# Optimization experiments

Hardware: AMD Instinct MI355X
Metric: run time of the kernel (lower is better)

## Reference

```python
import jax, jax.numpy as jnp
import numpy as np

N_NODES = 100000


def _gcn_norm(edge_index, num_nodes):
    # PyG GCNConv default: add self-loops, symmetric normalization.
    src = jnp.concatenate([edge_index[0], jnp.arange(num_nodes, dtype=edge_index.dtype)])
    dst = jnp.concatenate([edge_index[1], jnp.arange(num_nodes, dtype=edge_index.dtype)])
    deg = jax.ops.segment_sum(jnp.ones_like(dst, dtype=jnp.float32), dst, num_segments=num_nodes)
    dis = jnp.where(deg > 0, jax.lax.rsqrt(deg), 0.0)  # deg^{-1/2}
    norm = dis[src] * dis[dst]  # [E + N]
    return src, dst, norm


def _gcn_conv(x, W, b, src, dst, norm, num_nodes):
    h = x @ W.T                      # [N, out] transform first (out < in)
    msg = h[src] * norm[:, None]     # gather + per-edge scale
    agg = jax.ops.segment_sum(msg, dst, num_segments=num_nodes)  # scatter-add
    return agg + b


def setup_inputs() -> dict:
    key = jax.random.key(0)
    ks = jax.random.split(key, 12)
    E = 3200000
    x = jax.random.normal(ks[0], (N_NODES, 128), dtype=jnp.float32)
    edge_index = jax.random.randint(ks[1], (2, E), 0, N_NODES, dtype=jnp.int64)
    s = lambda k, sh, fan: jax.random.normal(k, sh, dtype=jnp.float32) * (1.0 / np.sqrt(fan))
    return {
        "x": x,
        "edge_index": edge_index,
        "W1": s(ks[2], (32, 128), 128), "b1": jnp.zeros((32,), jnp.float32),
        "W2": s(ks[3], (16, 32), 32),   "b2": jnp.zeros((16,), jnp.float32),
        "w_ih": s(ks[4], (32, 16), 16), "w_hh": s(ks[5], (32, 8), 8),
        "b_ih": s(ks[6], (32,), 8),     "b_hh": s(ks[7], (32,), 8),
        "W_out": s(ks[8], (1, 8), 8),   "b_out": jnp.zeros((1,), jnp.float32),
    }


def reference(x, edge_index, W1, b1, W2, b2, w_ih, w_hh, b_ih, b_hh, W_out, b_out):
    src, dst, norm = _gcn_norm(edge_index, N_NODES)
    h = jax.nn.relu(_gcn_conv(x, W1, b1, src, dst, norm, N_NODES))   # [N, 32]
    h = jax.nn.relu(_gcn_conv(h, W2, b2, src, dst, norm, N_NODES))   # [N, 16]
    # Single-timestep LSTM with h0 = c0 = 0 (gate order: i, f, g, o).
    gates = h @ w_ih.T + b_ih + b_hh   # [N, 32]; h0 @ w_hh.T term is zero
    i, f, g, o = jnp.split(gates, 4, axis=-1)
    c = jax.nn.sigmoid(i) * jnp.tanh(g)
    hh = jax.nn.sigmoid(o) * jnp.tanh(c)  # [N, 8]
    out = hh @ W_out.T + b_out            # [N, 1]
    return out.squeeze(-1)                # [N]
```

## Files before the change

### kernel.cpp

```cpp
#include <hip/hip_runtime.h>
#include <hip/hip_fp16.h>
#include <math.h>

static constexpr int N = 100000;
static constexpr int SHIFT = 7;
static constexpr int BUCKN = 1 << SHIFT;
static constexpr int NBUCK = (N + BUCKN - 1) >> SHIFT;
static constexpr int CHUNK = 12288;
static constexpr int STRIDE = 5120;
static constexpr int COLCAP = NBUCK * STRIDE;

__global__ __launch_bounds__(1024) void k_init(int* __restrict__ gcur) {
    int b = threadIdx.x;
    if (b < NBUCK) gcur[b] = b * STRIDE;
}

__global__ __launch_bounds__(1024) void k_part(const int* __restrict__ src,
                                               const int* __restrict__ dst,
                                               int* __restrict__ gcur,
                                               int* __restrict__ col, int E) {
    __shared__ int ss[CHUNK];
    __shared__ int ds[CHUNK];
    __shared__ int hl[NBUCK];
    __shared__ int cur[NBUCK];
    const int t = threadIdx.x, b = blockIdx.x;
    if (t < NBUCK) hl[t] = 0;
    __syncthreads();
    const int e0 = b * CHUNK;
    const int m = min(CHUNK, E - e0);
    for (int i = t; i < m; i += 1024) {
        int d = dst[e0 + i], s = src[e0 + i];
        ss[i] = s;
        ds[i] = d;
        atomicAdd(&hl[d >> SHIFT], 1);
    }
    __syncthreads();
    if (t < NBUCK) cur[t] = atomicAdd(&gcur[t], hl[t]);
    __syncthreads();
    for (int i = t; i < m; i += 1024) {
        int d = ds[i];
        int pos = atomicAdd(&cur[d >> SHIFT], 1);
        pos = min(max(pos, 0), COLCAP - 1);
        col[pos] = (ss[i] & 0x1FFFF) | ((d & (BUCKN - 1)) << 17);
    }
}

__global__ __launch_bounds__(1024) void k_sort(const int* __restrict__ gcur,
                                               int* __restrict__ col,
                                               int* __restrict__ deg,
                                               int* __restrict__ row_start) {
    __shared__ int es[STRIDE];
    __shared__ int cnt[BUCKN];
    __shared__ int cur[BUCKN];
    const int t = threadIdx.x, buck = blockIdx.x;
    const int s0 = buck * STRIDE;
    int n = gcur[buck] - s0;
    n = max(0, min(n, STRIDE));
    if (t < BUCKN) cnt[t] = 0;
    __syncthreads();
    for (int i = t; i < n; i += 1024) {
        int p = col[s0 + i];
        es[i] = p;
        atomicAdd(&cnt[(p >> 17) & (BUCKN - 1)], 1);
    }
    __syncthreads();
    if (t < BUCKN) cur[t] = cnt[t];
    __syncthreads();
    for (int off = 1; off < BUCKN; off <<= 1) {
        int v = (t < BUCKN && t >= off) ? cur[t - off] : 0;
        __syncthreads();
        if (t < BUCKN) cur[t] += v;
        __syncthreads();
    }
    if (t < BUCKN) {
        int excl = cur[t] - cnt[t];
        int node = buck * BUCKN + t;
        if (node < N) {
            deg[node] = cnt[t];
            row_start[node] = s0 + excl;
        }
        cur[t] = excl;
    }
    __syncthreads();
    for (int i = t; i < n; i += 1024) {
        int p = es[i];
        int pos = atomicAdd(&cur[(p >> 17) & (BUCKN - 1)], 1);
        pos = min(max(pos, 0), STRIDE - 1);
        col[s0 + pos] = p & 0x1FFFF;
    }
}

__global__ __launch_bounds__(256) void k_xw1(
        const float* __restrict__ x, const float* __restrict__ W1,
        const int* __restrict__ deg, __half* __restrict__ g1h) {
    __shared__ float4 wtv[32 * 33];
    __shared__ float4 xsv[1024];
    const int t = threadIdx.x;
    const float4* W1v = (const float4*)W1;
    for (int idx = t; idx < 1024; idx += 256) {
        int j = idx >> 5, kb = idx & 31;
        wtv[kb * 33 + j] = W1v[idx];
    }
    const float4* x4 = (const float4*)x + (size_t)blockIdx.x * 1024;
    for (int idx = t; idx < 1024; idx += 256) xsv[idx] = x4[idx];
    __syncthreads();

    const int j = t & 31, ng = t >> 5;
    float a0 = 0.f, a1 = 0.f, a2 = 0.f, a3 = 0.f;
#pragma unroll 4
    for (int kb = 0; kb < 32; ++kb) {
        float4 w = wtv[kb * 33 + j];
        float4 x0 = xsv[(4 * ng + 0) * 32 + kb];
        float4 x1 = xsv[(4 * ng + 1) * 32 + kb];
        float4 x2 = xsv[(4 * ng + 2) * 32 + kb];
        float4 x3 = xsv[(4 * ng + 3) * 32 + kb];
        a0 = fmaf(w.x, x0.x, fmaf(w.y, x0.y, fmaf(w.z, x0.z, fmaf(w.w, x0.w, a0))));
        a1 = fmaf(w.x, x1.x, fmaf(w.y, x1.y, fmaf(w.z, x1.z, fmaf(w.w, x1.w, a1))));
        a2 = fmaf(w.x, x2.x, fmaf(w.y, x2.y, fmaf(w.z, x2.z, fmaf(w.w, x2.w, a2))));
        a3 = fmaf(w.x, x3.x, fmaf(w.y, x3.y, fmaf(w.z, x3.z, fmaf(w.w, x3.w, a3))));
    }
    const int nb = blockIdx.x * 32 + 4 * ng;
    g1h[(nb + 0) * 32 + j] = __float2half(a0 * rsqrtf((float)(deg[nb + 0] + 1)));
    g1h[(nb + 1) * 32 + j] = __float2half(a1 * rsqrtf((float)(deg[nb + 1] + 1)));
    g1h[(nb + 2) * 32 + j] = __float2half(a2 * rsqrtf((float)(deg[nb + 2] + 1)));
    g1h[(nb + 3) * 32 + j] = __float2half(a3 * rsqrtf((float)(deg[nb + 3] + 1)));
}

__global__ __launch_bounds__(256) void k_gather1(
        const int* __restrict__ row_start, const int* __restrict__ deg,
        const int* __restrict__ col, const __half* __restrict__ g1h,
        const float* __restrict__ b1, const float* __restrict__ W2,
        __half* __restrict__ g2h) {
    __shared__ float h1s[64 * 33];
    __shared__ float w2t[32 * 17];
    const int t = threadIdx.x;
    for (int idx = t; idx < 512; idx += 256) {
        int j = idx >> 5, k = idx & 31;
        w2t[k * 17 + j] = W2[idx];
    }
    const int lane = t & 63, w = t >> 6;
    const int q = lane & 3;
    const int nloc = w * 16 + (lane >> 2);
    const int node = blockIdx.x * 64 + nloc;
    const int nc = node < N ? node : N - 1;
    const int rs = row_start[nc];
    const int ne = (node < N) ? deg[nc] : 0;
    const uint4* g1v = (const uint4*)g1h;

    float acc[8];
    {
        uint4 rv = g1v[nc * 4 + q];
        const __half2* hp = (const __half2*)&rv;
#pragma unroll
        for (int m2 = 0; m2 < 4; ++m2) {
            float2 f = __half22float2(hp[m2]);
            acc[2 * m2] = f.x;
            acc[2 * m2 + 1] = f.y;
        }
    }
    for (int base = 0; base < ne; base += 16) {
        int sv[4];
#pragma unroll
        for (int c = 0; c < 4; ++c)
            sv[c] = (base + 4 * c + q < ne) ? col[rs + base + 4 * c + q] : 0;
        int idx[16];
#pragma unroll
        for (int c = 0; c < 4; ++c)
#pragma unroll
            for (int u = 0; u < 4; ++u)
                idx[4 * c + u] = min(__shfl(sv[c], u, 4), N - 1);
        uint4 rv[16];
#pragma unroll
        for (int u = 0; u < 16; ++u) rv[u] = g1v[idx[u] * 4 + q];
#pragma unroll
        for (int u = 0; u < 16; ++u) {
            float wt = (base + u < ne) ? 1.f : 0.f;
            const __half2* hp = (const __half2*)&rv[u];
#pragma unroll
            for (int m2 = 0; m2 < 4; ++m2) {
                float2 f = __half22float2(hp[m2]);
                acc[2 * m2]     = fmaf(wt, f.x, acc[2 * m2]);
                acc[2 * m2 + 1] = fmaf(wt, f.y, acc[2 * m2 + 1]);
            }
        }
    }
    {
        const float dis = rsqrtf((float)(ne + 1));
#pragma unroll
        for (int u = 0; u < 8; ++u) {
            float v = (node < N) ? (acc[u] * dis + b1[q * 8 + u]) : 0.f;
            h1s[nloc * 33 + q * 8 + u] = v > 0.f ? v : 0.f;
        }
    }
    __syncthreads();
    const int n2 = t >> 2, jq = (t & 3) * 4;
    const int node2 = blockIdx.x * 64 + n2;
    if (node2 < N) {
        float a0 = 0.f, a1 = 0.f, a2 = 0.f, a3 = 0.f;
        const float* hr = h1s + n2 * 33;
#pragma unroll
        for (int k = 0; k < 32; ++k) {
            float h = hr[k];
            a0 = fmaf(h, w2t[k * 17 + jq + 0], a0);
            a1 = fmaf(h, w2t[k * 17 + jq + 1], a1);
            a2 = fmaf(h, w2t[k * 17 + jq + 2], a2);
            a3 = fmaf(h, w2t[k * 17 + jq + 3], a3);
        }
        const float dis2 = rsqrtf((float)(deg[node2] + 1));
        __half2* g2p = (__half2*)(g2h + node2 * 16 + jq);
        g2p[0] = __floats2half2_rn(a0 * dis2, a1 * dis2);
        g2p[1] = __floats2half2_rn(a2 * dis2, a3 * dis2);
    }
}

__global__ __launch_bounds__(256) void k_gather2(
        const int* __restrict__ row_start, const int* __restrict__ deg,
        const int* __restrict__ col, const __half* __restrict__ g2h,
        const float* __restrict__ b2, float* __restrict__ h2) {
    const int t = threadIdx.x;
    const int lane = t & 63, w = t >> 6;
    const int q = lane & 1;
    const int node = blockIdx.x * 128 + w * 32 + (lane >> 1);
    const int nc = node < N ? node : N - 1;
    const int rs = row_start[nc];
    const int ne = (node < N) ? deg[nc] : 0;
    const uint4* g2v = (const uint4*)g2h;

    float acc[8];
    {
        uint4 rv = g2v[nc * 2 + q];
        const __half2* hp = (const __half2*)&rv;
#pragma unroll
        for (int m2 = 0; m2 < 4; ++m2) {
            float2 f = __half22float2(hp[m2]);
            acc[2 * m2] = f.x;
            acc[2 * m2 + 1] = f.y;
        }
    }
    for (int base = 0; base < ne; base += 16) {
        int sv[8];
#pragma unroll
        for (int c = 0; c < 8; ++c)
            sv[c] = (base + 2 * c + q < ne) ? col[rs + base + 2 * c + q] : 0;
        int idx[16];
#pragma unroll
        for (int c = 0; c < 8; ++c) {
            idx[2 * c]     = min(__shfl(sv[c], 0, 2), N - 1);
            idx[2 * c + 1] = min(__shfl(sv[c], 1, 2), N - 1);
        }
        uint4 rv[16];
#pragma unroll
        for (int u = 0; u < 16; ++u) rv[u] = g2v[idx[u] * 2 + q];
#pragma unroll
        for (int u = 0; u < 16; ++u) {
            float wt = (base + u < ne) ? 1.f : 0.f;
            const __half2* hp = (const __half2*)&rv[u];
#pragma unroll
            for (int m2 = 0; m2 < 4; ++m2) {
                float2 f = __half22float2(hp[m2]);
                acc[2 * m2]     = fmaf(wt, f.x, acc[2 * m2]);
                acc[2 * m2 + 1] = fmaf(wt, f.y, acc[2 * m2 + 1]);
            }
        }
    }
    if (node < N) {
        const float dis = rsqrtf((float)(ne + 1));
        float4* h2v = (float4*)h2;
#pragma unroll
        for (int h = 0; h < 2; ++h) {
            float4 o;
            float v0 = acc[4 * h + 0] * dis + b2[q * 8 + 4 * h + 0];
            float v1 = acc[4 * h + 1] * dis + b2[q * 8 + 4 * h + 1];
            float v2 = acc[4 * h + 2] * dis + b2[q * 8 + 4 * h + 2];
            float v3 = acc[4 * h + 3] * dis + b2[q * 8 + 4 * h + 3];
            o.x = v0 > 0.f ? v0 : 0.f;
            o.y = v1 > 0.f ? v1 : 0.f;
            o.z = v2 > 0.f ? v2 : 0.f;
            o.w = v3 > 0.f ? v3 : 0.f;
            h2v[node * 4 + q * 2 + h] = o;
        }
    }
}

__global__ __launch_bounds__(256) void k_final(
        const float* __restrict__ h2g,
        const float* __restrict__ w_ih, const float* __restrict__ b_ih,
        const float* __restrict__ b_hh, const float* __restrict__ W_out,
        const float* __restrict__ b_out, float* __restrict__ out) {
    __shared__ float wih[512];
    __shared__ float bias[32];
    __shared__ float wout[8];
    __shared__ float bo;
    const int t = threadIdx.x;
    for (int idx = t; idx < 512; idx += 256) wih[idx] = w_ih[idx];
    if (t < 32) bias[t] = b_ih[t] + b_hh[t];
    if (t < 8)  wout[t] = W_out[t];
    if (t == 0) bo = b_out[0];
    __syncthreads();

    const int i = blockIdx.x * 256 + t;
    if (i >= N) return;
    float h2[16];
    const float4* a4 = (const float4*)(h2g + (size_t)i * 16);
#pragma unroll
    for (int q = 0; q < 4; ++q) {
        float4 v = a4[q];
        h2[q * 4 + 0] = v.x; h2[q * 4 + 1] = v.y;
        h2[q * 4 + 2] = v.z; h2[q * 4 + 3] = v.w;
    }
    float oacc = 0.f;
#pragma unroll
    for (int q = 0; q < 8; ++q) {
        float gi = bias[q], gg = bias[16 + q], go = bias[24 + q];
#pragma unroll
        for (int k = 0; k < 16; ++k) {
            gi = fmaf(h2[k], wih[q * 16 + k], gi);
            gg = fmaf(h2[k], wih[(16 + q) * 16 + k], gg);
            go = fmaf(h2[k], wih[(24 + q) * 16 + k], go);
        }
        float c  = (1.f / (1.f + expf(-gi))) * tanhf(gg);
        float hh = (1.f / (1.f + expf(-go))) * tanhf(c);
        oacc = fmaf(hh, wout[q], oacc);
    }
    out[i] = oacc + bo;
}

extern "C" void kernel_launch(void* const* d_in, const int* in_sizes, int n_in,
                              void* d_out, int out_size, void* d_ws, size_t ws_size,
                              hipStream_t stream) {
    const float* x     = (const float*)d_in[0];
    const int*   ei    = (const int*)d_in[1];
    const float* W1    = (const float*)d_in[2];
    const float* b1    = (const float*)d_in[3];
    const float* W2    = (const float*)d_in[4];
    const float* b2    = (const float*)d_in[5];
    const float* w_ih  = (const float*)d_in[6];
    const float* b_ih  = (const float*)d_in[8];
    const float* b_hh  = (const float*)d_in[9];
    const float* W_out = (const float*)d_in[10];
    const float* b_out = (const float*)d_in[11];
    float* out = (float*)d_out;

    const int E = in_sizes[1] / 2;
    const int* src = ei;
    const int* dst = ei + E;
    const int BP = (E + CHUNK - 1) / CHUNK;

    int* col       = (int*)d_ws;
    int* deg       = col + COLCAP;
    int* row_start = deg + N;
    int* gcur      = row_start + N;
    int* base2     = gcur + 784;
    __half* g1h    = (__half*)base2;
    __half* g2h    = (__half*)(base2 + (size_t)N * 16);
    float* h2      = (float*)(base2 + (size_t)N * 24);

    k_init   <<<1,               1024, 0, stream>>>(gcur);
    k_part   <<<BP,              1024, 0, stream>>>(src, dst, gcur, col, E);
    k_sort   <<<NBUCK,           1024, 0, stream>>>(gcur, col, deg, row_start);
    k_xw1    <<<N / 32,          256,  0, stream>>>(x, W1, deg, g1h);
    k_gather1<<<(N + 63) / 64,   256,  0, stream>>>(row_start, deg, col, g1h, b1, W2, g2h);
    k_gather2<<<(N + 127) / 128, 256,  0, stream>>>(row_start, deg, col, g2h, b2, h2);
    k_final  <<<(N + 255) / 256, 256,  0, stream>>>(h2, w_ih, b_ih, b_hh, W_out, b_out, out);
}
```

Measured before the change: 264.2 us.

## Fuse LSTM head into second gather and stream partition reads from global

```diff
diff --git a/kernel.cpp b/kernel.cpp
--- a/kernel.cpp
+++ b/kernel.cpp
@@ -6,7 +6,7 @@
 static constexpr int SHIFT = 7;
 static constexpr int BUCKN = 1 << SHIFT;
 static constexpr int NBUCK = (N + BUCKN - 1) >> SHIFT;
-static constexpr int CHUNK = 12288;
+static constexpr int CHUNK = 16384;
 static constexpr int STRIDE = 5120;
 static constexpr int COLCAP = NBUCK * STRIDE;
 
@@ -19,8 +19,6 @@
                                                const int* __restrict__ dst,
                                                int* __restrict__ gcur,
                                                int* __restrict__ col, int E) {
-    __shared__ int ss[CHUNK];
-    __shared__ int ds[CHUNK];
     __shared__ int hl[NBUCK];
     __shared__ int cur[NBUCK];
     const int t = threadIdx.x, b = blockIdx.x;
@@ -28,20 +26,15 @@
     __syncthreads();
     const int e0 = b * CHUNK;
     const int m = min(CHUNK, E - e0);
+    for (int i = t; i < m; i += 1024) atomicAdd(&hl[dst[e0 + i] >> SHIFT], 1);
+    __syncthreads();
+    if (t < NBUCK) cur[t] = atomicAdd(&gcur[t], hl[t]);
+    __syncthreads();
     for (int i = t; i < m; i += 1024) {
-        int d = dst[e0 + i], s = src[e0 + i];
-        ss[i] = s;
-        ds[i] = d;
-        atomicAdd(&hl[d >> SHIFT], 1);
-    }
-    __syncthreads();
-    if (t < NBUCK) cur[t] = atomicAdd(&gcur[t], hl[t]);
-    __syncthreads();
-    for (int i = t; i < m; i += 1024) {
-        int d = ds[i];
+        int d = dst[e0 + i];
         int pos = atomicAdd(&cur[d >> SHIFT], 1);
         pos = min(max(pos, 0), COLCAP - 1);
-        col[pos] = (ss[i] & 0x1FFFF) | ((d & (BUCKN - 1)) << 17);
+        col[pos] = (src[e0 + i] & 0x1FFFF) | ((d & (BUCKN - 1)) << 17);
     }
 }
 
@@ -216,77 +209,11 @@
 __global__ __launch_bounds__(256) void k_gather2(
         const int* __restrict__ row_start, const int* __restrict__ deg,
         const int* __restrict__ col, const __half* __restrict__ g2h,
-        const float* __restrict__ b2, float* __restrict__ h2) {
-    const int t = threadIdx.x;
-    const int lane = t & 63, w = t >> 6;
-    const int q = lane & 1;
-    const int node = blockIdx.x * 128 + w * 32 + (lane >> 1);
-    const int nc = node < N ? node : N - 1;
-    const int rs = row_start[nc];
-    const int ne = (node < N) ? deg[nc] : 0;
-    const uint4* g2v = (const uint4*)g2h;
-
-    float acc[8];
-    {
-        uint4 rv = g2v[nc * 2 + q];
-        const __half2* hp = (const __half2*)&rv;
-#pragma unroll
-        for (int m2 = 0; m2 < 4; ++m2) {
-            float2 f = __half22float2(hp[m2]);
-            acc[2 * m2] = f.x;
-            acc[2 * m2 + 1] = f.y;
-        }
-    }
-    for (int base = 0; base < ne; base += 16) {
-        int sv[8];
-#pragma unroll
-        for (int c = 0; c < 8; ++c)
-            sv[c] = (base + 2 * c + q < ne) ? col[rs + base + 2 * c + q] : 0;
-        int idx[16];
-#pragma unroll
-        for (int c = 0; c < 8; ++c) {
-            idx[2 * c]     = min(__shfl(sv[c], 0, 2), N - 1);
-            idx[2 * c + 1] = min(__shfl(sv[c], 1, 2), N - 1);
-        }
-        uint4 rv[16];
-#pragma unroll
-        for (int u = 0; u < 16; ++u) rv[u] = g2v[idx[u] * 2 + q];
-#pragma unroll
-        for (int u = 0; u < 16; ++u) {
-            float wt = (base + u < ne) ? 1.f : 0.f;
-            const __half2* hp = (const __half2*)&rv[u];
-#pragma unroll
-            for (int m2 = 0; m2 < 4; ++m2) {
-                float2 f = __half22float2(hp[m2]);
-                acc[2 * m2]     = fmaf(wt, f.x, acc[2 * m2]);
-                acc[2 * m2 + 1] = fmaf(wt, f.y, acc[2 * m2 + 1]);
-            }
-        }
-    }
-    if (node < N) {
-        const float dis = rsqrtf((float)(ne + 1));
-        float4* h2v = (float4*)h2;
-#pragma unroll
-        for (int h = 0; h < 2; ++h) {
-            float4 o;
-            float v0 = acc[4 * h + 0] * dis + b2[q * 8 + 4 * h + 0];
-            float v1 = acc[4 * h + 1] * dis + b2[q * 8 + 4 * h + 1];
-            float v2 = acc[4 * h + 2] * dis + b2[q * 8 + 4 * h + 2];
-            float v3 = acc[4 * h + 3] * dis + b2[q * 8 + 4 * h + 3];
-            o.x = v0 > 0.f ? v0 : 0.f;
-            o.y = v1 > 0.f ? v1 : 0.f;
-            o.z = v2 > 0.f ? v2 : 0.f;
-            o.w = v3 > 0.f ? v3 : 0.f;
-            h2v[node * 4 + q * 2 + h] = o;
-        }
-    }
-}
-
-__global__ __launch_bounds__(256) void k_final(
-        const float* __restrict__ h2g,
+        const float* __restrict__ b2,
         const float* __restrict__ w_ih, const float* __restrict__ b_ih,
         const float* __restrict__ b_hh, const float* __restrict__ W_out,
         const float* __restrict__ b_out, float* __restrict__ out) {
+    __shared__ float h2s[128 * 17];
     __shared__ float wih[512];
     __shared__ float bias[32];
     __shared__ float wout[8];
@@ -296,33 +223,83 @@
     if (t < 32) bias[t] = b_ih[t] + b_hh[t];
     if (t < 8)  wout[t] = W_out[t];
     if (t == 0) bo = b_out[0];
-    __syncthreads();
-
-    const int i = blockIdx.x * 256 + t;
-    if (i >= N) return;
-    float h2[16];
-    const float4* a4 = (const float4*)(h2g + (size_t)i * 16);
-#pragma unroll
-    for (int q = 0; q < 4; ++q) {
-        float4 v = a4[q];
-        h2[q * 4 + 0] = v.x; h2[q * 4 + 1] = v.y;
-        h2[q * 4 + 2] = v.z; h2[q * 4 + 3] = v.w;
-    }
-    float oacc = 0.f;
-#pragma unroll
-    for (int q = 0; q < 8; ++q) {
-        float gi = bias[q], gg = bias[16 + q], go = bias[24 + q];
-#pragma unroll
-        for (int k = 0; k < 16; ++k) {
-            gi = fmaf(h2[k], wih[q * 16 + k], gi);
-            gg = fmaf(h2[k], wih[(16 + q) * 16 + k], gg);
-            go = fmaf(h2[k], wih[(24 + q) * 16 + k], go);
-        }
-        float c  = (1.f / (1.f + expf(-gi))) * tanhf(gg);
-        float hh = (1.f / (1.f + expf(-go))) * tanhf(c);
-        oacc = fmaf(hh, wout[q], oacc);
-    }
-    out[i] = oacc + bo;
+
+    const int lane = t & 63, w = t >> 6;
+    const int q = lane & 1;
+    const int nloc = w * 32 + (lane >> 1);
+    const int node = blockIdx.x * 128 + nloc;
+    const int nc = node < N ? node : N - 1;
+    const int rs = row_start[nc];
+    const int ne = (node < N) ? deg[nc] : 0;
+    const uint4* g2v = (const uint4*)g2h;
+
+    float acc[8];
+    {
+        uint4 rv = g2v[nc * 2 + q];
+        const __half2* hp = (const __half2*)&rv;
+#pragma unroll
+        for (int m2 = 0; m2 < 4; ++m2) {
+            float2 f = __half22float2(hp[m2]);
+            acc[2 * m2] = f.x;
+            acc[2 * m2 + 1] = f.y;
+        }
+    }
+    for (int base = 0; base < ne; base += 16) {
+        int sv[8];
+#pragma unroll
+        for (int c = 0; c < 8; ++c)
+            sv[c] = (base + 2 * c + q < ne) ? col[rs + base + 2 * c + q] : 0;
+        int idx[16];
+#pragma unroll
+        for (int c = 0; c < 8; ++c) {
+            idx[2 * c]     = min(__shfl(sv[c], 0, 2), N - 1);
+            idx[2 * c + 1] = min(__shfl(sv[c], 1, 2), N - 1);
+        }
+        uint4 rv[16];
+#pragma unroll
+        for (int u = 0; u < 16; ++u) rv[u] = g2v[idx[u] * 2 + q];
+#pragma unroll
+        for (int u = 0; u < 16; ++u) {
+            float wt = (base + u < ne) ? 1.f : 0.f;
+            const __half2* hp = (const __half2*)&rv[u];
+#pragma unroll
+            for (int m2 = 0; m2 < 4; ++m2) {
+                float2 f = __half22float2(hp[m2]);
+                acc[2 * m2]     = fmaf(wt, f.x, acc[2 * m2]);
+                acc[2 * m2 + 1] = fmaf(wt, f.y, acc[2 * m2 + 1]);
+            }
+        }
+    }
+    {
+        const float dis = rsqrtf((float)(ne + 1));
+#pragma unroll
+        for (int u = 0; u < 8; ++u) {
+            float v = (node < N) ? (acc[u] * dis + b2[q * 8 + u]) : 0.f;
+            h2s[nloc * 17 + q * 8 + u] = v > 0.f ? v : 0.f;
+        }
+    }
+    __syncthreads();
+    if (t < 128) {
+        const int node2 = blockIdx.x * 128 + t;
+        if (node2 < N) {
+            const float* h2 = h2s + t * 17;
+            float oacc = 0.f;
+#pragma unroll
+            for (int g = 0; g < 8; ++g) {
+                float gi = bias[g], gg = bias[16 + g], go = bias[24 + g];
+#pragma unroll
+                for (int k = 0; k < 16; ++k) {
+                    gi = fmaf(h2[k], wih[g * 16 + k], gi);
+                    gg = fmaf(h2[k], wih[(16 + g) * 16 + k], gg);
+                    go = fmaf(h2[k], wih[(24 + g) * 16 + k], go);
+                }
+                float c  = (1.f / (1.f + expf(-gi))) * tanhf(gg);
+                float hh = (1.f / (1.f + expf(-go))) * tanhf(c);
+                oacc = fmaf(hh, wout[g], oacc);
+            }
+            out[node2] = oacc + bo;
+        }
+    }
 }
 
 extern "C" void kernel_launch(void* const* d_in, const int* in_sizes, int n_in,
@@ -353,13 +330,12 @@
     int* base2     = gcur + 784;
     __half* g1h    = (__half*)base2;
     __half* g2h    = (__half*)(base2 + (size_t)N * 16);
-    float* h2      = (float*)(base2 + (size_t)N * 24);
 
     k_init   <<<1,               1024, 0, stream>>>(gcur);
     k_part   <<<BP,              1024, 0, stream>>>(src, dst, gcur, col, E);
     k_sort   <<<NBUCK,           1024, 0, stream>>>(gcur, col, deg, row_start);
     k_xw1    <<<N / 32,          256,  0, stream>>>(x, W1, deg, g1h);
     k_gather1<<<(N + 63) / 64,   256,  0, stream>>>(row_start, deg, col, g1h, b1, W2, g2h);
-    k_gather2<<<(N + 127) / 128, 256,  0, stream>>>(row_start, deg, col, g2h, b2, h2);
-    k_final  <<<(N + 255) / 256, 256,  0, stream>>>(h2, w_ih, b_ih, b_hh, W_out, b_out, out);
-}
+    k_gather2<<<(N + 127) / 128, 256,  0, stream>>>(row_start, deg, col, g2h, b2,
+                                                    w_ih, b_ih, b_hh, W_out, b_out, out);
+}
```

Result: no change. 266.4 us (+0.8%).
